# Kernel optimization log

Hardware: AMD Instinct MI355X
Metric: run time of the kernel (lower is better)

The kernel has to match this reference:

```python
import jax, jax.numpy as jnp
import numpy as np
import math

B, L, D, H, FF = 32, 512, 512, 8, 2048
DH = D // H
EPS = 1e-5

def pe_table(L, D):
    pos = jnp.arange(L, dtype=jnp.float32)[:, None]
    div = jnp.exp(jnp.arange(0, D, 2, dtype=jnp.float32) * (-(math.log(10000.0) / D)))
    pe = jnp.zeros((L, D), dtype=jnp.float32)
    pe = pe.at[:, 0::2].set(jnp.sin(pos * div))
    pe = pe.at[:, 1::2].set(jnp.cos(pos * div))
    return pe

def setup_inputs() -> dict:
    key = jax.random.key(0)
    ks = jax.random.split(key, 16)
    s = 0.02
    inp = {
        "x": jax.random.normal(ks[0], (B, L, D), jnp.float32),
        "mask": jnp.ones((B, L), jnp.int32),
        "speaker_emb": jax.random.normal(ks[1], (B, L, D), jnp.float32),
        "Wg": jax.random.normal(ks[2], (D, D), jnp.float32) * s,
        "Wq": jax.random.normal(ks[3], (D, D), jnp.float32) * s,
        "bq": jnp.zeros((D,), jnp.float32),
        "Wk": jax.random.normal(ks[4], (D, D), jnp.float32) * s,
        "bk": jnp.zeros((D,), jnp.float32),
        "Wv": jax.random.normal(ks[5], (D, D), jnp.float32) * s,
        "bv": jnp.zeros((D,), jnp.float32),
        "Wo": jax.random.normal(ks[6], (D, D), jnp.float32) * s,
        "bo": jnp.zeros((D,), jnp.float32),
        "ln_g": jnp.ones((D,), jnp.float32),
        "ln_b": jnp.zeros((D,), jnp.float32),
        "W1": jax.random.normal(ks[7], (FF, D), jnp.float32) * s,
        "b1": jnp.zeros((FF,), jnp.float32),
        "W2": jax.random.normal(ks[8], (D, FF), jnp.float32) * s,
        "b2": jnp.zeros((D,), jnp.float32),
    }
    return inp

def layer_norm(x, g, b):
    mu = jnp.mean(x, axis=-1, keepdims=True)
    var = jnp.var(x, axis=-1, keepdims=True)
    return (x - mu) * jax.lax.rsqrt(var + EPS) * g + b

def reference(x, mask, speaker_emb, Wg, Wq, bq, Wk, bk, Wv, bv, Wo, bo, ln_g, ln_b, W1, b1, W2, b2):
    # DynamicGating: sigmoid(x W^T) * x
    x = jax.nn.sigmoid(x @ Wg.T) * x
    # speaker embedding + sinusoidal positional encoding (dropout is eval/no-op)
    x = x + speaker_emb + pe_table(L, D)[None, :, :]
    # Multi-head self-attention (eager, full score matrix)
    q = (x @ Wq.T + bq).reshape(B, L, H, DH).transpose(0, 2, 1, 3) / math.sqrt(DH)
    k = (x @ Wk.T + bk).reshape(B, L, H, DH).transpose(0, 2, 1, 3)
    v = (x @ Wv.T + bv).reshape(B, L, H, DH).transpose(0, 2, 1, 3)
    scores = jnp.einsum("bhqd,bhkd->bhqk", q, k)  # (B,H,L,L)
    key_mask = (mask == 0)[:, None, None, :]  # mask keys where mask==0
    scores = jnp.where(key_mask, jnp.float32(-1e10), scores)
    attn = jax.nn.softmax(scores, axis=-1)
    ctx = jnp.einsum("bhqk,bhkd->bhqd", attn, v)
    ctx = ctx.transpose(0, 2, 1, 3).reshape(B, L, D)
    attn_out = ctx @ Wo.T + bo
    h = attn_out + x  # residual (dropout no-op)
    # FeedForwardNet: note GELU applied after BOTH linears (faithful to source)
    mid = jax.nn.gelu(layer_norm(h, ln_g, ln_b) @ W1.T + b1, approximate=True)
    out = jax.nn.gelu(mid @ W2.T + b2, approximate=True)
    return out + h
```

## Files before the change

kernel.cpp:

```cpp
#include <hip/hip_runtime.h>
#include <math.h>

#define Bn 32
#define Ln 512
#define Dn 512
#define Hn 8
#define DHn 64
#define FFn 2048
#define Mn (Bn*Ln)
#define QKVS 1536

typedef __attribute__((ext_vector_type(4))) float f32x4;
typedef __attribute__((ext_vector_type(8))) short short8;

__device__ __forceinline__ float bf2f(ushort u){ return __uint_as_float(((unsigned)u) << 16); }
__device__ __forceinline__ ushort f2bf(float f){
  unsigned u = __float_as_uint(f);
  u += 0x7FFFu + ((u >> 16) & 1u);
  return (ushort)(u >> 16);
}
__device__ __forceinline__ float gelu_fast(float x){
  float y2 = 1.5957691216057308f * (x + 0.044715f*x*x*x);
  return x / (1.0f + __expf(-y2));
}

__device__ __forceinline__ void gload_lds16(const ushort* g, ushort* l){
  __builtin_amdgcn_global_load_lds(
      (__attribute__((address_space(1))) void*)(void*)g,
      (__attribute__((address_space(3))) void*)(void*)l, 16, 0, 0);
}

__global__ void pe_kernel(float* __restrict__ pe){
  int idx = blockIdx.x*256 + threadIdx.x;
  if (idx >= Ln*Dn) return;
  int l = idx / Dn, d = idx - l*Dn;
  int i = d >> 1;
  float dv = expf((float)(2*i) * (-logf(10000.0f)/(float)Dn));
  float ang = (float)l * dv;
  pe[idx] = (d & 1) ? cosf(ang) : sinf(ang);
}

__global__ void cvt_kernel(const float* __restrict__ in, ushort* __restrict__ out, int n){
  int i = (blockIdx.x*256 + threadIdx.x)*4;
  if (i >= n) return;
  float4 v = *(const float4*)(in + i);
  ushort4 o;
  o.x = f2bf(v.x); o.y = f2bf(v.y); o.z = f2bf(v.z); o.w = f2bf(v.w);
  *(ushort4*)(out + i) = o;
}

__global__ void pack_bias_kernel(const float* __restrict__ bq, const float* __restrict__ bk,
                                 const float* __restrict__ bv, float* __restrict__ out){
  int i = blockIdx.x*256 + threadIdx.x;
  if (i >= QKVS) return;
  out[i] = (i < 512) ? bq[i] : (i < 1024) ? bk[i-512] : bv[i-1024];
}

template<int MODE>
__global__ __launch_bounds__(256) void gemm_kernel(
    const ushort* __restrict__ A, const ushort* __restrict__ W,
    const float* __restrict__ bias,
    const float* __restrict__ res,
    const float* __restrict__ spk, const float* __restrict__ pe,
    float* __restrict__ outf, ushort* __restrict__ outb,
    int K, int N, int gx)
{
  __shared__ ushort lA[128][64];
  __shared__ ushort lW[128][64];
  int t = threadIdx.x;
  int wave = t >> 6, lane = t & 63;
  int wr = wave >> 1, wc = wave & 1;
  int g = lane >> 4, r16 = lane & 15;

  int nwg = gx << 7;
  int wg = blockIdx.x;
  int tile = (wg & 7)*(nwg >> 3) + (wg >> 3);
  int trow = tile / gx;
  int tcol = tile - trow*gx;
  int rowBase = trow * 128;
  int colBase = tcol * 128;

  int srow8 = lane >> 3;
  int sucol = ((lane & 7) ^ srow8) * 8;
  const ushort* gA = A + (size_t)(rowBase + wave*8 + srow8)*K + sucol;
  const ushort* gW = W + (size_t)(colBase + wave*8 + srow8)*K + sucol;
  ushort* lAbase = &lA[0][0] + wave*512;
  ushort* lWbase = &lW[0][0] + wave*512;

  f32x4 acc[4][4];
  #pragma unroll
  for (int m=0;m<4;m++)
    #pragma unroll
    for (int n=0;n<4;n++) acc[m][n] = (f32x4)0.0f;

  for (int k0 = 0; k0 < K; k0 += 64){
    #pragma unroll
    for (int c=0;c<4;c++){
      gload_lds16(gA + (size_t)c*32*K + k0, lAbase + c*2048);
      gload_lds16(gW + (size_t)c*32*K + k0, lWbase + c*2048);
    }
    __syncthreads();
    #pragma unroll
    for (int ks=0; ks<2; ks++){
      short8 af[4], bfr[4];
      #pragma unroll
      for (int m=0;m<4;m++){
        int row = wr*64 + m*16 + r16;
        af[m] = *(const short8*)&lA[row][(((ks<<2)+g) ^ (r16 & 7))*8];
      }
      #pragma unroll
      for (int n=0;n<4;n++){
        int row = wc*64 + n*16 + r16;
        bfr[n] = *(const short8*)&lW[row][(((ks<<2)+g) ^ (r16 & 7))*8];
      }
      #pragma unroll
      for (int m=0;m<4;m++)
        #pragma unroll
        for (int n=0;n<4;n++)
          acc[m][n] = __builtin_amdgcn_mfma_f32_16x16x32_bf16(af[m], bfr[n], acc[m][n], 0, 0, 0);
    }
    __syncthreads();
  }

  #pragma unroll
  for (int m=0;m<4;m++){
    #pragma unroll
    for (int n=0;n<4;n++){
      #pragma unroll
      for (int j=0;j<4;j++){
        int gr = rowBase + wr*64 + m*16 + g*4 + j;
        int gc = colBase + wc*64 + n*16 + r16;
        size_t o = (size_t)gr * N + gc;
        float c = acc[m][n][j];
        if constexpr (MODE == 0){
          float s = 1.0f/(1.0f + __expf(-c));
          float rv = s * res[o] + spk[o] + pe[(gr & (Ln-1))*Dn + gc];
          outf[o] = rv; outb[o] = f2bf(rv);
        } else if constexpr (MODE == 1){
          float sc = (gc < 512) ? 0.125f : 1.0f;
          outb[o] = f2bf((c + bias[gc]) * sc);
        } else if constexpr (MODE == 2){
          outf[o] = c + bias[gc] + res[o];
        } else if constexpr (MODE == 3){
          outb[o] = f2bf(gelu_fast(c + bias[gc]));
        } else {
          outf[o] = gelu_fast(c + bias[gc]) + res[o];
        }
      }
    }
  }
}

__global__ __launch_bounds__(256) void attn_mfma_kernel(
    const ushort* __restrict__ qb, const ushort* __restrict__ kb, const ushort* __restrict__ vb,
    const int* __restrict__ mask, ushort* __restrict__ ctxb)
{
  __shared__ ushort lK[64][72];
  __shared__ ushort lVt[64][72];
  __shared__ ushort lP[4][32][72];

  int t = threadIdx.x;
  int w = t >> 6, lane = t & 63;
  int g = lane >> 4, r16 = lane & 15;
  int b = blockIdx.z, h = blockIdx.y;
  int qbase = blockIdx.x*128 + w*32;

  short8 af_q[2][2];
  #pragma unroll
  for (int m=0;m<2;m++)
    #pragma unroll
    for (int ks=0;ks<2;ks++)
      af_q[m][ks] = *(const short8*)(qb + (size_t)(b*Ln + qbase + m*16 + r16)*QKVS + h*DHn + ks*32 + g*8);

  f32x4 acc_ctx[2][4];
  #pragma unroll
  for (int m=0;m<2;m++)
    #pragma unroll
    for (int n=0;n<4;n++) acc_ctx[m][n] = (f32x4)0.0f;
  float mrun[2][4], lrun[2][4];
  #pragma unroll
  for (int m=0;m<2;m++)
    #pragma unroll
    for (int j=0;j<4;j++){ mrun[m][j] = -INFINITY; lrun[m][j] = 0.0f; }

  for (int kb0 = 0; kb0 < Ln; kb0 += 64){
    __syncthreads();
    #pragma unroll
    for (int i=0;i<2;i++){
      int cid = t + i*256;
      int key = cid >> 3, c8 = (cid & 7)*8;
      short8 kv = *(const short8*)(kb + (size_t)(b*Ln + kb0 + key)*QKVS + h*DHn + c8);
      short8 vv = *(const short8*)(vb + (size_t)(b*Ln + kb0 + key)*QKVS + h*DHn + c8);
      *(short8*)&lK[key][c8] = kv;
      #pragma unroll
      for (int j=0;j<8;j++){
        int row = c8 + j;
        int colp = (key & 7) + 8*((key >> 3) ^ ((row >> 3) & 7));
        lVt[row][colp] = (ushort)vv[j];
      }
    }
    __syncthreads();

    f32x4 acc_s[2][4];
    #pragma unroll
    for (int m=0;m<2;m++)
      #pragma unroll
      for (int n=0;n<4;n++) acc_s[m][n] = (f32x4)0.0f;
    __builtin_amdgcn_s_setprio(1);
    #pragma unroll
    for (int ks=0;ks<2;ks++){
      short8 bf_k[4];
      #pragma unroll
      for (int n=0;n<4;n++)
        bf_k[n] = *(const short8*)&lK[n*16 + r16][ks*32 + g*8];
      #pragma unroll
      for (int m=0;m<2;m++)
        #pragma unroll
        for (int n=0;n<4;n++)
          acc_s[m][n] = __builtin_amdgcn_mfma_f32_16x16x32_bf16(af_q[m][ks], bf_k[n], acc_s[m][n], 0, 0, 0);
    }
    __builtin_amdgcn_s_setprio(0);

    #pragma unroll
    for (int n=0;n<4;n++){
      if (mask[b*Ln + kb0 + n*16 + r16] == 0){
        #pragma unroll
        for (int m=0;m<2;m++)
          #pragma unroll
          for (int j=0;j<4;j++) acc_s[m][n][j] = -1e10f;
      }
    }

    #pragma unroll
    for (int m=0;m<2;m++){
      #pragma unroll
      for (int j=0;j<4;j++){
        float tmax = fmaxf(fmaxf(acc_s[m][0][j], acc_s[m][1][j]),
                           fmaxf(acc_s[m][2][j], acc_s[m][3][j]));
        #pragma unroll
        for (int off=1; off<16; off<<=1) tmax = fmaxf(tmax, __shfl_xor(tmax, off));
        float newm = fmaxf(mrun[m][j], tmax);
        float alpha = __expf(mrun[m][j] - newm);
        float p0 = __expf(acc_s[m][0][j] - newm);
        float p1 = __expf(acc_s[m][1][j] - newm);
        float p2 = __expf(acc_s[m][2][j] - newm);
        float p3 = __expf(acc_s[m][3][j] - newm);
        float tsum = (p0+p1)+(p2+p3);
        #pragma unroll
        for (int off=1; off<16; off<<=1) tsum += __shfl_xor(tsum, off);
        lrun[m][j] = lrun[m][j]*alpha + tsum;
        mrun[m][j] = newm;
        #pragma unroll
        for (int n2=0;n2<4;n2++) acc_ctx[m][n2][j] *= alpha;
        int prow = m*16 + g*4 + j;
        lP[w][prow][0*16 + r16] = f2bf(p0);
        lP[w][prow][1*16 + r16] = f2bf(p1);
        lP[w][prow][2*16 + r16] = f2bf(p2);
        lP[w][prow][3*16 + r16] = f2bf(p3);
      }
    }

    __builtin_amdgcn_s_setprio(1);
    #pragma unroll
    for (int ks2=0;ks2<2;ks2++){
      short8 af_p[2], bf_v[4];
      #pragma unroll
      for (int m=0;m<2;m++)
        af_p[m] = *(const short8*)&lP[w][m*16 + r16][ks2*32 + g*8];
      #pragma unroll
      for (int n=0;n<4;n++){
        int vrow = n*16 + r16;
        int blk = ((ks2*32 + g*8) >> 3) ^ ((vrow >> 3) & 7);
        bf_v[n] = *(const short8*)&lVt[vrow][blk*8];
      }
      #pragma unroll
      for (int m=0;m<2;m++)
        #pragma unroll
        for (int n=0;n<4;n++)
          acc_ctx[m][n] = __builtin_amdgcn_mfma_f32_16x16x32_bf16(af_p[m], bf_v[n], acc_ctx[m][n], 0, 0, 0);
    }
    __builtin_amdgcn_s_setprio(0);
  }

  #pragma unroll
  for (int m=0;m<2;m++){
    #pragma unroll
    for (int j=0;j<4;j++){
      float inv = 1.0f / lrun[m][j];
      int gr = qbase + m*16 + g*4 + j;
      #pragma unroll
      for (int n=0;n<4;n++){
        ctxb[(size_t)(b*Ln + gr)*Dn + h*DHn + n*16 + r16] = f2bf(acc_ctx[m][n][j] * inv);
      }
    }
  }
}

__global__ __launch_bounds__(256) void ln_kernel(
    const float* __restrict__ hbuf, const float* __restrict__ gamma, const float* __restrict__ beta,
    ushort* __restrict__ out)
{
  int row = blockIdx.x*4 + (threadIdx.x >> 6);
  int lane = threadIdx.x & 63;
  const float* p = hbuf + (size_t)row*Dn + lane*8;
  float4 a = *(const float4*)p;
  float4 c = *(const float4*)(p + 4);
  float v[8] = {a.x,a.y,a.z,a.w,c.x,c.y,c.z,c.w};
  float s = 0.f, ss = 0.f;
  #pragma unroll
  for (int j=0;j<8;j++){ s += v[j]; ss += v[j]*v[j]; }
  #pragma unroll
  for (int off=32; off>0; off>>=1){ s += __shfl_xor(s, off); ss += __shfl_xor(ss, off); }
  float mu = s * (1.0f/Dn);
  float var = ss * (1.0f/Dn) - mu*mu;
  float rstd = rsqrtf(var + 1e-5f);
  ushort o8[8];
  #pragma unroll
  for (int j=0;j<8;j++) o8[j] = f2bf((v[j]-mu)*rstd*gamma[lane*8+j] + beta[lane*8+j]);
  ushort* op = out + (size_t)row*Dn + lane*8;
  *(ushort4*)op       = make_ushort4(o8[0],o8[1],o8[2],o8[3]);
  *(ushort4*)(op + 4) = make_ushort4(o8[4],o8[5],o8[6],o8[7]);
}

extern "C" void kernel_launch(void* const* d_in, const int* in_sizes, int n_in,
                              void* d_out, int out_size, void* d_ws, size_t ws_size,
                              hipStream_t stream) {
  (void)in_sizes; (void)n_in; (void)out_size; (void)ws_size;
  const float* x    = (const float*)d_in[0];
  const int*   mask = (const int*)d_in[1];
  const float* spk  = (const float*)d_in[2];
  const float* Wg   = (const float*)d_in[3];
  const float* Wq   = (const float*)d_in[4];  const float* bq = (const float*)d_in[5];
  const float* Wk   = (const float*)d_in[6];  const float* bk = (const float*)d_in[7];
  const float* Wv   = (const float*)d_in[8];  const float* bv = (const float*)d_in[9];
  const float* Wo   = (const float*)d_in[10]; const float* bo = (const float*)d_in[11];
  const float* lng  = (const float*)d_in[12]; const float* lnbeta = (const float*)d_in[13];
  const float* W1   = (const float*)d_in[14]; const float* b1 = (const float*)d_in[15];
  const float* W2   = (const float*)d_in[16]; const float* b2 = (const float*)d_in[17];
  float* out = (float*)d_out;

  char* w = (char*)d_ws;
  size_t o = 0;
  ushort* xbf   = (ushort*)(w + o); o += (size_t)Mn*Dn*2;
  ushort* xinb  = (ushort*)(w + o); o += (size_t)Mn*Dn*2;
  ushort* qkvb  = (ushort*)(w + o); o += (size_t)Mn*QKVS*2;
  ushort* ctxb  = (ushort*)(w + o); o += (size_t)Mn*Dn*2;
  float*  xinf  = (float*)(w + o);  o += (size_t)Mn*Dn*4;
  float*  hbuf  = (float*)(w + o);  o += (size_t)Mn*Dn*4;
  ushort* lnbuf = (ushort*)(w + o); o += (size_t)Mn*Dn*2;
  ushort* wgb   = (ushort*)(w + o); o += (size_t)Dn*Dn*2;
  ushort* wqkvb = (ushort*)(w + o); o += (size_t)QKVS*Dn*2;
  ushort* wob   = (ushort*)(w + o); o += (size_t)Dn*Dn*2;
  ushort* w1b   = (ushort*)(w + o); o += (size_t)FFn*Dn*2;
  ushort* w2b   = (ushort*)(w + o); o += (size_t)Dn*FFn*2;
  float*  pebuf = (float*)(w + o);  o += (size_t)Ln*Dn*4;
  float*  bqkv  = (float*)(w + o);  o += (size_t)QKVS*4;
  ushort* midb  = xbf;

  hipLaunchKernelGGL(pe_kernel, dim3((Ln*Dn)/256), dim3(256), 0, stream, pebuf);
  hipLaunchKernelGGL(cvt_kernel, dim3((Mn*Dn/4)/256), dim3(256), 0, stream, x, xbf, Mn*Dn);
  hipLaunchKernelGGL(cvt_kernel, dim3((Dn*Dn/4)/256), dim3(256), 0, stream, Wg, wgb, Dn*Dn);
  hipLaunchKernelGGL(cvt_kernel, dim3((Dn*Dn/4)/256), dim3(256), 0, stream, Wq, wqkvb,            Dn*Dn);
  hipLaunchKernelGGL(cvt_kernel, dim3((Dn*Dn/4)/256), dim3(256), 0, stream, Wk, wqkvb + Dn*Dn,    Dn*Dn);
  hipLaunchKernelGGL(cvt_kernel, dim3((Dn*Dn/4)/256), dim3(256), 0, stream, Wv, wqkvb + 2*Dn*Dn,  Dn*Dn);
  hipLaunchKernelGGL(cvt_kernel, dim3((Dn*Dn/4)/256), dim3(256), 0, stream, Wo, wob, Dn*Dn);
  hipLaunchKernelGGL(cvt_kernel, dim3((FFn*Dn/4)/256), dim3(256), 0, stream, W1, w1b, FFn*Dn);
  hipLaunchKernelGGL(cvt_kernel, dim3((FFn*Dn/4)/256), dim3(256), 0, stream, W2, w2b, FFn*Dn);
  hipLaunchKernelGGL(pack_bias_kernel, dim3((QKVS+255)/256), dim3(256), 0, stream, bq, bk, bv, bqkv);

  hipLaunchKernelGGL((gemm_kernel<0>), dim3((Dn/128)*(Mn/128)), dim3(256), 0, stream,
                     xbf, wgb, (const float*)nullptr, x, spk, pebuf, xinf, xinb, Dn, Dn, Dn/128);
  hipLaunchKernelGGL((gemm_kernel<1>), dim3((QKVS/128)*(Mn/128)), dim3(256), 0, stream,
                     xinb, wqkvb, bqkv, (const float*)nullptr, (const float*)nullptr, (const float*)nullptr,
                     (float*)nullptr, qkvb, Dn, QKVS, QKVS/128);
  hipLaunchKernelGGL(attn_mfma_kernel, dim3(Ln/128, Hn, Bn), dim3(256), 0, stream,
                     qkvb, qkvb + 512, qkvb + 1024, mask, ctxb);
  hipLaunchKernelGGL((gemm_kernel<2>), dim3((Dn/128)*(Mn/128)), dim3(256), 0, stream,
                     ctxb, wob, bo, xinf, (const float*)nullptr, (const float*)nullptr,
                     hbuf, (ushort*)nullptr, Dn, Dn, Dn/128);
  hipLaunchKernelGGL(ln_kernel, dim3(Mn/4), dim3(256), 0, stream, hbuf, lng, lnbeta, lnbuf);
  hipLaunchKernelGGL((gemm_kernel<3>), dim3((FFn/128)*(Mn/128)), dim3(256), 0, stream,
                     lnbuf, w1b, b1, (const float*)nullptr, (const float*)nullptr, (const float*)nullptr,
                     (float*)nullptr, midb, Dn, FFn, FFn/128);
  hipLaunchKernelGGL((gemm_kernel<4>), dim3((Dn/128)*(Mn/128)), dim3(256), 0, stream,
                     midb, w2b, b2, hbuf, (const float*)nullptr, (const float*)nullptr,
                     out, (ushort*)nullptr, FFn, Dn, Dn/128);
}
```

Before: 318.8 us.

## Double-buffer GEMM and attention K loads, pre-transpose V, fuse prep kernels

The GEMM main loop gets double-buffered LDS with the next K-tile prefetched via global_load_lds during MFMA work. The QKV GEMM writes V in a transposed per-head layout, so attention reads V fragments straight from global memory and drops the per-element LDS transpose. K tiles in attention are register-prefetched into a second LDS buffer. The weight conversions, PE table and bias packing are merged into one prep launch. Costs are double the LDS per GEMM block, which may lower occupancy, and uncached global V reads inside the attention inner loop.

Result: no change. 319.0 us (+0.1%).

```diff
diff --git a/kernel.cpp b/kernel.cpp
--- a/kernel.cpp
+++ b/kernel.cpp
@@ -30,30 +30,58 @@
       (__attribute__((address_space(3))) void*)(void*)l, 16, 0, 0);
 }
 
-__global__ void pe_kernel(float* __restrict__ pe){
-  int idx = blockIdx.x*256 + threadIdx.x;
-  if (idx >= Ln*Dn) return;
-  int l = idx / Dn, d = idx - l*Dn;
-  int i = d >> 1;
-  float dv = expf((float)(2*i) * (-logf(10000.0f)/(float)Dn));
-  float ang = (float)l * dv;
-  pe[idx] = (d & 1) ? cosf(ang) : sinf(ang);
+__device__ __forceinline__ void cvt4(const float* __restrict__ in, ushort* __restrict__ out, int u){
+  float4 v = *(const float4*)(in + u*4);
+  ushort4 o;
+  o.x = f2bf(v.x); o.y = f2bf(v.y); o.z = f2bf(v.z); o.w = f2bf(v.w);
+  *(ushort4*)(out + u*4) = o;
+}
+
+__global__ __launch_bounds__(256) void prep_kernel(
+    const float* __restrict__ Wg, const float* __restrict__ Wq, const float* __restrict__ Wk,
+    const float* __restrict__ Wv, const float* __restrict__ Wo, const float* __restrict__ W1,
+    const float* __restrict__ W2,
+    const float* __restrict__ bq, const float* __restrict__ bk, const float* __restrict__ bv,
+    ushort* __restrict__ wgb, ushort* __restrict__ wqkvb, ushort* __restrict__ wob,
+    ushort* __restrict__ w1b, ushort* __restrict__ w2b,
+    float* __restrict__ pe, float* __restrict__ bqkv)
+{
+  int u = blockIdx.x*256 + threadIdx.x;
+  const int WU = 65536, FU = 262144;
+  if (u < WU){ cvt4(Wg, wgb, u); return; }            u -= WU;
+  if (u < WU){ cvt4(Wq, wqkvb, u); return; }          u -= WU;
+  if (u < WU){ cvt4(Wk, wqkvb + 262144, u); return; } u -= WU;
+  if (u < WU){ cvt4(Wv, wqkvb + 524288, u); return; } u -= WU;
+  if (u < WU){ cvt4(Wo, wob, u); return; }            u -= WU;
+  if (u < FU){ cvt4(W1, w1b, u); return; }            u -= FU;
+  if (u < FU){ cvt4(W2, w2b, u); return; }            u -= FU;
+  if (u < WU){
+    int e = u*4; int l = e >> 9; int d0 = e & 511;
+    #pragma unroll
+    for (int p=0;p<2;p++){
+      int i = (d0 >> 1) + p;
+      float dv = expf((float)(2*i) * (-9.210340371976184f/512.0f));
+      float ang = (float)l * dv;
+      pe[e + 2*p]     = sinf(ang);
+      pe[e + 2*p + 1] = cosf(ang);
+    }
+    return;
+  }
+  u -= WU;
+  if (u < 384){
+    int e = u*4;
+    #pragma unroll
+    for (int j=0;j<4;j++){
+      int i = e + j;
+      bqkv[i] = (i < 512) ? bq[i] : (i < 1024) ? bk[i-512] : bv[i-1024];
+    }
+  }
 }
 
 __global__ void cvt_kernel(const float* __restrict__ in, ushort* __restrict__ out, int n){
   int i = (blockIdx.x*256 + threadIdx.x)*4;
   if (i >= n) return;
-  float4 v = *(const float4*)(in + i);
-  ushort4 o;
-  o.x = f2bf(v.x); o.y = f2bf(v.y); o.z = f2bf(v.z); o.w = f2bf(v.w);
-  *(ushort4*)(out + i) = o;
-}
-
-__global__ void pack_bias_kernel(const float* __restrict__ bq, const float* __restrict__ bk,
-                                 const float* __restrict__ bv, float* __restrict__ out){
-  int i = blockIdx.x*256 + threadIdx.x;
-  if (i >= QKVS) return;
-  out[i] = (i < 512) ? bq[i] : (i < 1024) ? bk[i-512] : bv[i-1024];
+  cvt4(in, out, i >> 2);
 }
 
 template<int MODE>
@@ -62,17 +90,17 @@
     const float* __restrict__ bias,
     const float* __restrict__ res,
     const float* __restrict__ spk, const float* __restrict__ pe,
-    float* __restrict__ outf, ushort* __restrict__ outb,
+    float* __restrict__ outf, ushort* __restrict__ outb, ushort* __restrict__ outb2,
     int K, int N, int gx)
 {
-  __shared__ ushort lA[128][64];
-  __shared__ ushort lW[128][64];
+  __shared__ ushort lA[2][128][64];
+  __shared__ ushort lW[2][128][64];
   int t = threadIdx.x;
   int wave = t >> 6, lane = t & 63;
   int wr = wave >> 1, wc = wave & 1;
   int g = lane >> 4, r16 = lane & 15;
 
-  int nwg = gx << 7;
+  int nwg = gx * (Mn/128);
   int wg = blockIdx.x;
   int tile = (wg & 7)*(nwg >> 3) + (wg >> 3);
   int trow = tile / gx;
@@ -84,8 +112,6 @@
   int sucol = ((lane & 7) ^ srow8) * 8;
   const ushort* gA = A + (size_t)(rowBase + wave*8 + srow8)*K + sucol;
   const ushort* gW = W + (size_t)(colBase + wave*8 + srow8)*K + sucol;
-  ushort* lAbase = &lA[0][0] + wave*512;
-  ushort* lWbase = &lW[0][0] + wave*512;
 
   f32x4 acc[4][4];
   #pragma unroll
@@ -93,25 +119,40 @@
     #pragma unroll
     for (int n=0;n<4;n++) acc[m][n] = (f32x4)0.0f;
 
+  {
+    ushort* la = &lA[0][0][0] + wave*512;
+    ushort* lw = &lW[0][0][0] + wave*512;
+    #pragma unroll
+    for (int c=0;c<4;c++){
+      gload_lds16(gA + (size_t)c*32*K, la + c*2048);
+      gload_lds16(gW + (size_t)c*32*K, lw + c*2048);
+    }
+  }
+  __syncthreads();
+
+  int cb = 0;
   for (int k0 = 0; k0 < K; k0 += 64){
-    #pragma unroll
-    for (int c=0;c<4;c++){
-      gload_lds16(gA + (size_t)c*32*K + k0, lAbase + c*2048);
-      gload_lds16(gW + (size_t)c*32*K + k0, lWbase + c*2048);
-    }
-    __syncthreads();
+    if (k0 + 64 < K){
+      ushort* la = &lA[cb^1][0][0] + wave*512;
+      ushort* lw = &lW[cb^1][0][0] + wave*512;
+      #pragma unroll
+      for (int c=0;c<4;c++){
+        gload_lds16(gA + (size_t)c*32*K + k0 + 64, la + c*2048);
+        gload_lds16(gW + (size_t)c*32*K + k0 + 64, lw + c*2048);
+      }
+    }
     #pragma unroll
     for (int ks=0; ks<2; ks++){
       short8 af[4], bfr[4];
       #pragma unroll
       for (int m=0;m<4;m++){
         int row = wr*64 + m*16 + r16;
-        af[m] = *(const short8*)&lA[row][(((ks<<2)+g) ^ (r16 & 7))*8];
+        af[m] = *(const short8*)&lA[cb][row][(((ks<<2)+g) ^ (r16 & 7))*8];
       }
       #pragma unroll
       for (int n=0;n<4;n++){
         int row = wc*64 + n*16 + r16;
-        bfr[n] = *(const short8*)&lW[row][(((ks<<2)+g) ^ (r16 & 7))*8];
+        bfr[n] = *(const short8*)&lW[cb][row][(((ks<<2)+g) ^ (r16 & 7))*8];
       }
       #pragma unroll
       for (int m=0;m<4;m++)
@@ -120,43 +161,61 @@
           acc[m][n] = __builtin_amdgcn_mfma_f32_16x16x32_bf16(af[m], bfr[n], acc[m][n], 0, 0, 0);
     }
     __syncthreads();
+    cb ^= 1;
   }
 
   #pragma unroll
   for (int m=0;m<4;m++){
     #pragma unroll
     for (int n=0;n<4;n++){
-      #pragma unroll
-      for (int j=0;j<4;j++){
-        int gr = rowBase + wr*64 + m*16 + g*4 + j;
-        int gc = colBase + wc*64 + n*16 + r16;
-        size_t o = (size_t)gr * N + gc;
-        float c = acc[m][n][j];
-        if constexpr (MODE == 0){
-          float s = 1.0f/(1.0f + __expf(-c));
-          float rv = s * res[o] + spk[o] + pe[(gr & (Ln-1))*Dn + gc];
-          outf[o] = rv; outb[o] = f2bf(rv);
-        } else if constexpr (MODE == 1){
+      int gc = colBase + wc*64 + n*16 + r16;
+      if constexpr (MODE == 1){
+        if (gc < 1024){
           float sc = (gc < 512) ? 0.125f : 1.0f;
-          outb[o] = f2bf((c + bias[gc]) * sc);
-        } else if constexpr (MODE == 2){
-          outf[o] = c + bias[gc] + res[o];
-        } else if constexpr (MODE == 3){
-          outb[o] = f2bf(gelu_fast(c + bias[gc]));
+          #pragma unroll
+          for (int j=0;j<4;j++){
+            int gr = rowBase + wr*64 + m*16 + g*4 + j;
+            outb[(size_t)gr*N + gc] = f2bf((acc[m][n][j] + bias[gc]) * sc);
+          }
         } else {
-          outf[o] = gelu_fast(c + bias[gc]) + res[o];
+          int dhg = gc - 1024;
+          int gr0 = rowBase + wr*64 + m*16 + g*4;
+          int bb = gr0 >> 9, l0 = gr0 & 511;
+          ushort4 o4;
+          o4.x = f2bf(acc[m][n][0] + bias[gc]);
+          o4.y = f2bf(acc[m][n][1] + bias[gc]);
+          o4.z = f2bf(acc[m][n][2] + bias[gc]);
+          o4.w = f2bf(acc[m][n][3] + bias[gc]);
+          *(ushort4*)(outb2 + ((size_t)(bb*Hn + (dhg>>6))*DHn + (dhg & 63))*Ln + l0) = o4;
         }
+      } else {
+        #pragma unroll
+        for (int j=0;j<4;j++){
+          int gr = rowBase + wr*64 + m*16 + g*4 + j;
+          size_t o = (size_t)gr * N + gc;
+          float c = acc[m][n][j];
+          if constexpr (MODE == 0){
+            float s = 1.0f/(1.0f + __expf(-c));
+            float rv = s * res[o] + spk[o] + pe[(gr & (Ln-1))*Dn + gc];
+            outf[o] = rv; outb[o] = f2bf(rv);
+          } else if constexpr (MODE == 2){
+            outf[o] = c + bias[gc] + res[o];
+          } else if constexpr (MODE == 3){
+            outb[o] = f2bf(gelu_fast(c + bias[gc]));
+          } else {
+            outf[o] = gelu_fast(c + bias[gc]) + res[o];
+          }
+        }
       }
     }
   }
 }
 
 __global__ __launch_bounds__(256) void attn_mfma_kernel(
-    const ushort* __restrict__ qb, const ushort* __restrict__ kb, const ushort* __restrict__ vb,
+    const ushort* __restrict__ qb, const ushort* __restrict__ kb, const ushort* __restrict__ vtb,
     const int* __restrict__ mask, ushort* __restrict__ ctxb)
 {
-  __shared__ ushort lK[64][72];
-  __shared__ ushort lVt[64][72];
+  __shared__ ushort lK[2][64][72];
   __shared__ ushort lP[4][32][72];
 
   int t = threadIdx.x;
@@ -165,6 +224,11 @@
   int b = blockIdx.z, h = blockIdx.y;
   int qbase = blockIdx.x*128 + w*32;
 
+  int key0 = t >> 3, key1 = key0 + 32;
+  int c8s = (t & 7) * 8;
+  const ushort* kbase = kb + (size_t)(b*Ln)*QKVS + h*DHn + c8s;
+  const ushort* vt = vtb + (size_t)((b*Hn + h)*DHn) * Ln;
+
   short8 af_q[2][2];
   #pragma unroll
   for (int m=0;m<2;m++)
@@ -183,23 +247,22 @@
     #pragma unroll
     for (int j=0;j<4;j++){ mrun[m][j] = -INFINITY; lrun[m][j] = 0.0f; }
 
+  {
+    short8 ka = *(const short8*)(kbase + (size_t)key0*QKVS);
+    short8 kc = *(const short8*)(kbase + (size_t)key1*QKVS);
+    *(short8*)&lK[0][key0][c8s] = ka;
+    *(short8*)&lK[0][key1][c8s] = kc;
+  }
+  __syncthreads();
+  int cb = 0;
+
   for (int kb0 = 0; kb0 < Ln; kb0 += 64){
-    __syncthreads();
-    #pragma unroll
-    for (int i=0;i<2;i++){
-      int cid = t + i*256;
-      int key = cid >> 3, c8 = (cid & 7)*8;
-      short8 kv = *(const short8*)(kb + (size_t)(b*Ln + kb0 + key)*QKVS + h*DHn + c8);
-      short8 vv = *(const short8*)(vb + (size_t)(b*Ln + kb0 + key)*QKVS + h*DHn + c8);
-      *(short8*)&lK[key][c8] = kv;
-      #pragma unroll
-      for (int j=0;j<8;j++){
-        int row = c8 + j;
-        int colp = (key & 7) + 8*((key >> 3) ^ ((row >> 3) & 7));
-        lVt[row][colp] = (ushort)vv[j];
-      }
-    }
-    __syncthreads();
+    short8 kna, knb;
+    bool more = (kb0 + 64 < Ln);
+    if (more){
+      kna = *(const short8*)(kbase + (size_t)(kb0 + 64 + key0)*QKVS);
+      knb = *(const short8*)(kbase + (size_t)(kb0 + 64 + key1)*QKVS);
+    }
 
     f32x4 acc_s[2][4];
     #pragma unroll
@@ -212,7 +275,7 @@
       short8 bf_k[4];
       #pragma unroll
       for (int n=0;n<4;n++)
-        bf_k[n] = *(const short8*)&lK[n*16 + r16][ks*32 + g*8];
+        bf_k[n] = *(const short8*)&lK[cb][n*16 + r16][ks*32 + g*8];
       #pragma unroll
       for (int m=0;m<2;m++)
         #pragma unroll
@@ -268,11 +331,8 @@
       for (int m=0;m<2;m++)
         af_p[m] = *(const short8*)&lP[w][m*16 + r16][ks2*32 + g*8];
       #pragma unroll
-      for (int n=0;n<4;n++){
-        int vrow = n*16 + r16;
-        int blk = ((ks2*32 + g*8) >> 3) ^ ((vrow >> 3) & 7);
-        bf_v[n] = *(const short8*)&lVt[vrow][blk*8];
-      }
+      for (int n=0;n<4;n++)
+        bf_v[n] = *(const short8*)(vt + (size_t)(n*16 + r16)*Ln + kb0 + ks2*32 + g*8);
       #pragma unroll
       for (int m=0;m<2;m++)
         #pragma unroll
@@ -280,6 +340,13 @@
           acc_ctx[m][n] = __builtin_amdgcn_mfma_f32_16x16x32_bf16(af_p[m], bf_v[n], acc_ctx[m][n], 0, 0, 0);
     }
     __builtin_amdgcn_s_setprio(0);
+
+    if (more){
+      *(short8*)&lK[cb^1][key0][c8s] = kna;
+      *(short8*)&lK[cb^1][key1][c8s] = knb;
+    }
+    __syncthreads();
+    cb ^= 1;
   }
 
   #pragma unroll
@@ -344,6 +411,7 @@
   ushort* xbf   = (ushort*)(w + o); o += (size_t)Mn*Dn*2;
   ushort* xinb  = (ushort*)(w + o); o += (size_t)Mn*Dn*2;
   ushort* qkvb  = (ushort*)(w + o); o += (size_t)Mn*QKVS*2;
+  ushort* vtb   = (ushort*)(w + o); o += (size_t)Mn*Dn*2;
   ushort* ctxb  = (ushort*)(w + o); o += (size_t)Mn*Dn*2;
   float*  xinf  = (float*)(w + o);  o += (size_t)Mn*Dn*4;
   float*  hbuf  = (float*)(w + o);  o += (size_t)Mn*Dn*4;
@@ -357,32 +425,27 @@
   float*  bqkv  = (float*)(w + o);  o += (size_t)QKVS*4;
   ushort* midb  = xbf;
 
-  hipLaunchKernelGGL(pe_kernel, dim3((Ln*Dn)/256), dim3(256), 0, stream, pebuf);
+  hipLaunchKernelGGL(prep_kernel, dim3(3586), dim3(256), 0, stream,
+                     Wg, Wq, Wk, Wv, Wo, W1, W2, bq, bk, bv,
+                     wgb, wqkvb, wob, w1b, w2b, pebuf, bqkv);
   hipLaunchKernelGGL(cvt_kernel, dim3((Mn*Dn/4)/256), dim3(256), 0, stream, x, xbf, Mn*Dn);
-  hipLaunchKernelGGL(cvt_kernel, dim3((Dn*Dn/4)/256), dim3(256), 0, stream, Wg, wgb, Dn*Dn);
-  hipLaunchKernelGGL(cvt_kernel, dim3((Dn*Dn/4)/256), dim3(256), 0, stream, Wq, wqkvb,            Dn*Dn);
-  hipLaunchKernelGGL(cvt_kernel, dim3((Dn*Dn/4)/256), dim3(256), 0, stream, Wk, wqkvb + Dn*Dn,    Dn*Dn);
-  hipLaunchKernelGGL(cvt_kernel, dim3((Dn*Dn/4)/256), dim3(256), 0, stream, Wv, wqkvb + 2*Dn*Dn,  Dn*Dn);
-  hipLaunchKernelGGL(cvt_kernel, dim3((Dn*Dn/4)/256), dim3(256), 0, stream, Wo, wob, Dn*Dn);
-  hipLaunchKernelGGL(cvt_kernel, dim3((FFn*Dn/4)/256), dim3(256), 0, stream, W1, w1b, FFn*Dn);
-  hipLaunchKernelGGL(cvt_kernel, dim3((FFn*Dn/4)/256), dim3(256), 0, stream, W2, w2b, FFn*Dn);
-  hipLaunchKernelGGL(pack_bias_kernel, dim3((QKVS+255)/256), dim3(256), 0, stream, bq, bk, bv, bqkv);
 
   hipLaunchKernelGGL((gemm_kernel<0>), dim3((Dn/128)*(Mn/128)), dim3(256), 0, stream,
-                     xbf, wgb, (const float*)nullptr, x, spk, pebuf, xinf, xinb, Dn, Dn, Dn/128);
+                     xbf, wgb, (const float*)nullptr, x, spk, pebuf, xinf, xinb, (ushort*)nullptr,
+                     Dn, Dn, Dn/128);
   hipLaunchKernelGGL((gemm_kernel<1>), dim3((QKVS/128)*(Mn/128)), dim3(256), 0, stream,
                      xinb, wqkvb, bqkv, (const float*)nullptr, (const float*)nullptr, (const float*)nullptr,
-                     (float*)nullptr, qkvb, Dn, QKVS, QKVS/128);
+                     (float*)nullptr, qkvb, vtb, Dn, QKVS, QKVS/128);
   hipLaunchKernelGGL(attn_mfma_kernel, dim3(Ln/128, Hn, Bn), dim3(256), 0, stream,
-                     qkvb, qkvb + 512, qkvb + 1024, mask, ctxb);
+                     qkvb, qkvb + 512, vtb, mask, ctxb);
   hipLaunchKernelGGL((gemm_kernel<2>), dim3((Dn/128)*(Mn/128)), dim3(256), 0, stream,
                      ctxb, wob, bo, xinf, (const float*)nullptr, (const float*)nullptr,
-                     hbuf, (ushort*)nullptr, Dn, Dn, Dn/128);
+                     hbuf, (ushort*)nullptr, (ushort*)nullptr, Dn, Dn, Dn/128);
   hipLaunchKernelGGL(ln_kernel, dim3(Mn/4), dim3(256), 0, stream, hbuf, lng, lnbeta, lnbuf);
   hipLaunchKernelGGL((gemm_kernel<3>), dim3((FFn/128)*(Mn/128)), dim3(256), 0, stream,
                      lnbuf, w1b, b1, (const float*)nullptr, (const float*)nullptr, (const float*)nullptr,
-                     (float*)nullptr, midb, Dn, FFn, FFn/128);
+                     (float*)nullptr, midb, (ushort*)nullptr, Dn, FFn, FFn/128);
   hipLaunchKernelGGL((gemm_kernel<4>), dim3((Dn/128)*(Mn/128)), dim3(256), 0, stream,
                      midb, w2b, b2, hbuf, (const float*)nullptr, (const float*)nullptr,
-                     out, (ushort*)nullptr, FFn, Dn, Dn/128);
-}
+                     out, (ushort*)nullptr, (ushort*)nullptr, FFn, Dn, Dn/128);
+}
```
